# Optimization experiments

Hardware: AMD Instinct MI355X
Metric: run time of the kernel (lower is better)

Reference implementation:

```python
import jax, jax.numpy as jnp
import numpy as np

WL_W = 8   # wl_weight
WL_IN = 8  # wl_activate (input quantization)
EPS = 1e-5

def _wq(x, bits):
    # WAGE-style uniform quantize-dequantize to `bits` bits in [-1+step, 1-step], STE passthrough
    step = 2.0 ** (1 - bits)
    q = jnp.clip(jnp.round(x / step) * step, -1.0 + step, 1.0 - step)
    return x + jax.lax.stop_gradient(q - x)

def _qconv(x, w, b, pad):
    y = jax.lax.conv_general_dilated(
        _wq(x, WL_IN), _wq(w, WL_W), (1, 1), [(pad, pad), (pad, pad)],
        dimension_numbers=('NCHW', 'OIHW', 'NCHW'))
    return y + b[None, :, None, None]

def _bn_relu(x, g, be):
    # BatchNorm2d in training mode: batch statistics over (N, H, W)
    m = jnp.mean(x, axis=(0, 2, 3), keepdims=True)
    v = jnp.var(x, axis=(0, 2, 3), keepdims=True)
    return jax.nn.relu((x - m) * jax.lax.rsqrt(v + EPS) * g[None, :, None, None] + be[None, :, None, None])

def _maxpool3(x):
    # MaxPool2d(3, stride=1, padding=1)
    return jax.lax.reduce_window(x, -jnp.inf, jax.lax.max,
                                 (1, 1, 3, 3), (1, 1, 1, 1),
                                 [(0, 0), (0, 0), (1, 1), (1, 1)])

def setup_inputs() -> dict:
    key = jax.random.key(0)
    ks = jax.random.split(key, 8)
    d = {'x': jax.random.normal(ks[0], (128, 192, 32, 32), jnp.float32)}
    specs = [('b1', 1, 64, 192, 1), ('b2a', 2, 96, 192, 1), ('b2b', 3, 128, 96, 3),
             ('b3a', 4, 16, 192, 1), ('b3b', 5, 32, 16, 3), ('b3c', 6, 32, 32, 3),
             ('b4', 7, 32, 192, 1)]
    for name, i, co, ci, k in specs:
        d[name + '_w'] = jax.random.normal(ks[i], (co, ci, k, k), jnp.float32) * 0.05
        d[name + '_b'] = jnp.zeros((co,), jnp.float32)
        d[name + '_g'] = jnp.ones((co,), jnp.float32)
        d[name + '_be'] = jnp.zeros((co,), jnp.float32)
    return d

def reference(x,
              b1_w, b1_b, b1_g, b1_be,
              b2a_w, b2a_b, b2a_g, b2a_be,
              b2b_w, b2b_b, b2b_g, b2b_be,
              b3a_w, b3a_b, b3a_g, b3a_be,
              b3b_w, b3b_b, b3b_g, b3b_be,
              b3c_w, b3c_b, b3c_g, b3c_be,
              b4_w, b4_b, b4_g, b4_be):
    y1 = _bn_relu(_qconv(x, b1_w, b1_b, 0), b1_g, b1_be)
    y2 = _bn_relu(_qconv(x, b2a_w, b2a_b, 0), b2a_g, b2a_be)
    y2 = _bn_relu(_qconv(y2, b2b_w, b2b_b, 1), b2b_g, b2b_be)
    y3 = _bn_relu(_qconv(x, b3a_w, b3a_b, 0), b3a_g, b3a_be)
    y3 = _bn_relu(_qconv(y3, b3b_w, b3b_b, 1), b3b_g, b3b_be)
    y3 = _bn_relu(_qconv(y3, b3c_w, b3c_b, 1), b3c_g, b3c_be)
    y4 = _bn_relu(_qconv(_maxpool3(x), b4_w, b4_b, 0), b4_g, b4_be)
    return jnp.concatenate([y1, y2, y3, y4], axis=1)  # [N, 256, 32, 32]
```

## Files before the change

kernel.cpp:

```cpp
#include <hip/hip_runtime.h>

typedef unsigned short u16;
typedef unsigned int u32;
typedef __attribute__((ext_vector_type(4))) int i32x4;
typedef __attribute__((ext_vector_type(4))) float f32x4;
typedef __attribute__((ext_vector_type(4))) u16 u16x4;
typedef __attribute__((ext_vector_type(8))) u16 u16x8;

#define PTOT 131072
#define NREP 16

static __device__ __forceinline__ int qi8(float v) {
  int q = (int)rintf(v * 128.f);
  return max(-127, min(127, q));
}
static __device__ __forceinline__ u16 bf_rne(float v) {
  u32 u = __float_as_uint(v);
  u += 0x7fffu + ((u >> 16) & 1u);
  return (u16)(u >> 16);
}
static __device__ __forceinline__ float bf2f(u16 v) {
  return __uint_as_float((u32)v << 16);
}

struct WPtrs { const float* p[7]; };

__global__ void wpack_kernel(WPtrs wp, char* __restrict__ o) {
  static const int S[7][5] = {
      {0,      192, 192, 1, 64},
      {12288,  192, 192, 1, 96},
      {30720,  96,  320, 3, 128},
      {153600, 192, 192, 1, 16},
      {156672, 16,  64,  3, 32},
      {162816, 32,  128, 3, 32},
      {175104, 192, 192, 1, 32},
  };
  int idx = blockIdx.x * 256 + threadIdx.x;
  if (idx >= 181248) return;
  int s = 0;
#pragma unroll
  for (int i = 1; i < 7; ++i)
    if (idx >= S[i][0]) s = i;
  int local = idx - S[s][0];
  int CIr = S[s][1], KROWP = S[s][2], KH = S[s][3], Co = S[s][4];
  int j = local & 15, lane = (local >> 4) & 63, f = local >> 10;
  int NF = Co >> 4;
  int c = f / NF, nf = f - c * NF;
  int co = nf * 16 + (lane & 15);
  int k = c * 64 + ((lane >> 4) << 4) + j;
  int r = k / KROWP, kk = k - r * KROWP;
  char val = 0;
  if (kk < 3 * CIr || KH == 1) {
    int kw = (KH == 1) ? 0 : (kk / CIr);
    int ci = (KH == 1) ? kk : (kk - kw * CIr);
    val = (char)qi8(wp.p[s][(((size_t)co * CIr + ci) * KH + r) * KH + kw]);
  }
  o[idx] = val;
}

__global__ __launch_bounds__(256) void quantx_kernel(const float* __restrict__ x,
                                                     char* __restrict__ xq) {
  __shared__ __align__(16) char tile[64][80];
  int n = blockIdx.z, hwb = blockIdx.x * 64, cb = blockIdx.y * 64;
  int lane = threadIdx.x & 63, sub = threadIdx.x >> 6;
#pragma unroll
  for (int i = 0; i < 16; ++i) {
    int c = sub + i * 4;
    float v = x[(((size_t)n * 192 + cb + c) << 10) + hwb + lane];
    tile[lane][c] = (char)qi8(v);
  }
  __syncthreads();
  int t = threadIdx.x, px = t >> 2, c16 = t & 3;
  uint4 v = *(const uint4*)&tile[px][c16 * 16];
  *(uint4*)&xq[(((size_t)n << 10) + hwb + px) * 192 + cb + c16 * 16] = v;
}

__global__ __launch_bounds__(256) void pool_kernel(const char* __restrict__ xq,
                                                   char* __restrict__ xpq) {
  int idx = blockIdx.x * 256 + threadIdx.x;
  int c16 = idx % 12;
  int p = idx / 12;
  int n = p >> 10, hw = p & 1023, h = hw >> 5, w = hw & 31;
  int m[16];
#pragma unroll
  for (int j = 0; j < 16; ++j) m[j] = -127;
  for (int dh = -1; dh <= 1; ++dh) {
    int hh = h + dh; if (hh < 0 || hh > 31) continue;
    for (int dw = -1; dw <= 1; ++dw) {
      int ww = w + dw; if (ww < 0 || ww > 31) continue;
      uint4 v = *(const uint4*)&xq[((((size_t)n << 5) + hh) * 32 + ww) * 192 + c16 * 16];
      const char* bb = reinterpret_cast<const char*>(&v);
#pragma unroll
      for (int t = 0; t < 16; ++t) {
        int b = (int)bb[t];
        m[t] = b > m[t] ? b : m[t];
      }
    }
  }
  uint4 o;
  char* ob = reinterpret_cast<char*>(&o);
#pragma unroll
  for (int t = 0; t < 16; ++t) ob[t] = (char)m[t];
  *(uint4*)&xpq[(size_t)p * 192 + c16 * 16] = o;
}

template <int NFW, int MF>
static __device__ __forceinline__ void conv_epilogue(
    i32x4 (&acc)[MF][NFW], int nfw, int lane, int wave, int mbase,
    u16* __restrict__ yh, double* __restrict__ stb, int ststride) {
  float yv[MF][NFW][4];
#pragma unroll
  for (int mf = 0; mf < MF; ++mf)
#pragma unroll
    for (int nf = 0; nf < NFW; ++nf)
      if (nf < nfw) {
        int col = nf * 16 + (lane & 15);
        int pix = mbase + mf * 16 + ((lane >> 4) << 2);
        u16x4 o;
#pragma unroll
        for (int r = 0; r < 4; ++r) {
          float v = (float)acc[mf][nf][r] * 6.103515625e-05f;
          yv[mf][nf][r] = v;
          o[r] = bf_rne(v);
        }
        *(u16x4*)&yh[(size_t)col * PTOT + pix] = o;
      }

  float s1[NFW], s2[NFW];
#pragma unroll
  for (int nf = 0; nf < NFW; ++nf) { s1[nf] = 0.f; s2[nf] = 0.f; }
#pragma unroll
  for (int mf = 0; mf < MF; ++mf)
#pragma unroll
    for (int nf = 0; nf < NFW; ++nf)
      if (nf < nfw)
#pragma unroll
        for (int r = 0; r < 4; ++r) {
          float v = yv[mf][nf][r];
          s1[nf] += v;
          s2[nf] += v * v;
        }
#pragma unroll
  for (int m = 16; m <= 32; m <<= 1)
#pragma unroll
    for (int nf = 0; nf < NFW; ++nf) {
      s1[nf] += __shfl_xor(s1[nf], m);
      s2[nf] += __shfl_xor(s2[nf], m);
    }
  __shared__ float red[4][NFW][16][2];
  if (lane < 16)
#pragma unroll
    for (int nf = 0; nf < NFW; ++nf) {
      red[wave][nf][lane][0] = s1[nf];
      red[wave][nf][lane][1] = s2[nf];
    }
  __syncthreads();
  const int t = threadIdx.x;
  if (t < 16 * nfw) {
    int nf = t >> 4, l = t & 15;
    float a = red[0][nf][l][0] + red[1][nf][l][0] + red[2][nf][l][0] + red[3][nf][l][0];
    float b = red[0][nf][l][1] + red[1][nf][l][1] + red[2][nf][l][1] + red[3][nf][l][1];
    int rep = blockIdx.x & (NREP - 1);
    atomicAdd(&stb[rep * ststride + 2 * t], (double)a);
    atomicAdd(&stb[rep * ststride + 2 * t + 1], (double)b);
  }
}

__global__ __launch_bounds__(256, 4) void cstat1x1_kernel(
    const char* __restrict__ xq, const char* __restrict__ xpq,
    const char* __restrict__ bpk, double* __restrict__ st, u16* __restrict__ yh) {
  constexpr int NFW = 6;
  constexpr int MF = 2;
  const int b = blockIdx.y;
  const int nfw = (b == 0) ? 4 : (b == 1) ? 6 : (b == 2) ? 1 : 2;
  const int bpo = (b == 0) ? 0 : (b == 1) ? 12288 : (b == 2) ? 153600 : 175104;
  const int sto = (b == 0) ? 0 : (b == 1) ? 256 * NREP
                           : (b == 2) ? 3 * 256 * NREP : 6 * 256 * NREP;
  const int yho = (b == 0) ? 0 : (b == 1) ? 64 : (b == 2) ? 160 : 176;
  const char* xin = (b == 3) ? xpq : xq;
  const char* bp = bpk + bpo;
  double* stb = st + sto;
  u16* yhb = yh + (size_t)yho * PTOT;

  const int lane = threadIdx.x & 63;
  const int wave = threadIdx.x >> 6;
  const int mbase = blockIdx.x * 128 + wave * 32;

  uint abase[MF];
#pragma unroll
  for (int mf = 0; mf < MF; ++mf)
    abase[mf] = (uint)(mbase + mf * 16 + (lane & 15)) * 192u;
  const uint klane = (uint)(lane >> 4) * 16u;
  const uint blane = (uint)lane * 16u;

  i32x4 acc[MF][NFW];
#pragma unroll
  for (int i = 0; i < MF; ++i)
#pragma unroll
    for (int j = 0; j < NFW; ++j) acc[i][j] = {0, 0, 0, 0};

#pragma unroll
  for (int c = 0; c < 3; ++c) {
    i32x4 af[MF];
#pragma unroll
    for (int mf = 0; mf < MF; ++mf)
      af[mf] = *(const i32x4*)(xin + (abase[mf] + (uint)c * 64u + klane));
    i32x4 bfr[NFW];
#pragma unroll
    for (int nf = 0; nf < NFW; ++nf)
      if (nf < nfw)
        bfr[nf] = *(const i32x4*)(bp + ((uint)((c * nfw + nf) * 1024) + blane));
#pragma unroll
    for (int mf = 0; mf < MF; ++mf)
#pragma unroll
      for (int nf = 0; nf < NFW; ++nf)
        if (nf < nfw)
          acc[mf][nf] = __builtin_amdgcn_mfma_i32_16x16x64_i8(af[mf], bfr[nf],
                                                              acc[mf][nf], 0, 0, 0);
  }

  conv_epilogue<NFW, MF>(acc, nfw, lane, wave, mbase, yhb, stb, 256);
}

template <int CI, int KROWP, int COB, int WPEU>
__global__ __launch_bounds__(256, WPEU) void cstat9q_kernel(
    const u16* __restrict__ yhin, const double* __restrict__ stp,
    const float* __restrict__ gp, const float* __restrict__ bep,
    const char* __restrict__ bp, int nft,
    double* __restrict__ stb, u16* __restrict__ yh) {
  constexpr int CPR = KROWP / 64;
  constexpr int NCH = 3 * CPR;
  constexpr int NFW = COB / 16;
  constexpr int MF = 2;
  constexpr int TILE = 6 * 34 * CI;

  __shared__ __align__(16) char atile[TILE + 64];
  __shared__ float2 cfl[CI];

  const int tid = threadIdx.x;

  if (tid < CI) {
    double s1d = 0., s2d = 0.;
#pragma unroll
    for (int r = 0; r < NREP; ++r) {
      s1d += stp[r * 256 + 2 * tid];
      s2d += stp[r * 256 + 2 * tid + 1];
    }
    double m = s1d * (1.0 / PTOT);
    double v = s2d * (1.0 / PTOT) - m * m;
    double inv = 1.0 / sqrt(v + 1e-5);
    double c0 = (double)gp[tid] * inv;
    cfl[tid] = make_float2((float)c0, (float)((double)bep[tid] - m * c0));
  }
  {
    uint4 z = {0, 0, 0, 0};
    for (int s = tid * 16; s < TILE + 64; s += 4096) *(uint4*)&atile[s] = z;
  }
  __syncthreads();

  const int p0 = blockIdx.x * 128;
  const int n = p0 >> 10, h0 = (p0 & 1023) >> 5;
  for (int task = tid; task < CI * 6; task += 256) {
    int co = task / 6, rr = task - co * 6;
    int irow = h0 - 1 + rr;
    if (irow < 0 || irow > 31) continue;
    const u16* src = yhin + (size_t)co * PTOT + (n << 10) + (irow << 5);
    float2 cc = cfl[co];
    char* dst = &atile[(rr * 34 + 1) * CI + co];
#pragma unroll
    for (int w8 = 0; w8 < 4; ++w8) {
      u16x8 v = *(const u16x8*)(src + w8 * 8);
#pragma unroll
      for (int e = 0; e < 8; ++e) {
        float z = fmaxf(fmaf(bf2f(v[e]), cc.x, cc.y), 0.f);
        dst[(w8 * 8 + e) * CI] = (char)min((int)rintf(z * 128.f), 127);
      }
    }
  }
  __syncthreads();

  const int lane = tid & 63;
  const int wave = tid >> 6;
  const int mbase = blockIdx.x * 128 + wave * 32;

  uint albase[MF];
#pragma unroll
  for (int mf = 0; mf < MF; ++mf) {
    int lp = wave * 32 + mf * 16 + (lane & 15);
    albase[mf] = (uint)((((lp >> 5) + 1) * 34 + 1 + (lp & 31)) * CI);
  }
  const uint klane = (uint)(lane >> 4) * 16u;
  const uint blane = (uint)lane * 16u;

  i32x4 acc[MF][NFW];
#pragma unroll
  for (int i = 0; i < MF; ++i)
#pragma unroll
    for (int j = 0; j < NFW; ++j) acc[i][j] = {0, 0, 0, 0};

#pragma unroll 2
  for (int c = 0; c < NCH; ++c) {
    int rr = c / CPR, o = (c - rr * CPR) * 64;
    uint koff = (uint)((rr - 1) * 34 * CI + o - CI);
    i32x4 af[MF];
#pragma unroll
    for (int mf = 0; mf < MF; ++mf)
      af[mf] = *(const i32x4*)&atile[albase[mf] + koff + klane];
    i32x4 bfr[NFW];
#pragma unroll
    for (int nf = 0; nf < NFW; ++nf)
      bfr[nf] = *(const i32x4*)(bp + ((uint)((c * nft + nf) * 1024) + blane));
#pragma unroll
    for (int mf = 0; mf < MF; ++mf)
#pragma unroll
      for (int nf = 0; nf < NFW; ++nf)
        acc[mf][nf] = __builtin_amdgcn_mfma_i32_16x16x64_i8(af[mf], bfr[nf],
                                                            acc[mf][nf], 0, 0, 0);
  }

  conv_epilogue<NFW, MF>(acc, NFW, lane, wave, mbase, yh, stb, 256);
}

struct BnPtrs { const float* g[4]; const float* be[4]; };

__global__ __launch_bounds__(256) void bnout_all_kernel(
    const u16* __restrict__ yh, const double* __restrict__ st, BnPtrs bp,
    float* __restrict__ out) {
  int co = blockIdx.y, chunk = blockIdx.x, tid = threadIdx.x;
  int br = (co < 64) ? 0 : (co < 192) ? 1 : (co < 224) ? 2 : 3;
  int lco = co - ((br == 0) ? 0 : (br == 1) ? 64 : (br == 2) ? 192 : 224);
  int yhoff = (br == 0) ? 0 : (br == 1) ? 208 : (br == 2) ? 368 : 176;
  int stoff = (br == 0) ? 0 : (br == 1) ? 2 * 256 * NREP
                         : (br == 2) ? 5 * 256 * NREP : 6 * 256 * NREP;
  const double* stb = st + stoff;
  double s1d = 0., s2d = 0.;
#pragma unroll
  for (int r = 0; r < NREP; ++r) {
    s1d += stb[r * 256 + 2 * lco];
    s2d += stb[r * 256 + 2 * lco + 1];
  }
  double m = s1d * (1.0 / PTOT);
  double v = s2d * (1.0 / PTOT) - m * m;
  double inv = 1.0 / sqrt(v + 1e-5);
  double c0d = (double)bp.g[br][lco] * inv;
  float c0 = (float)c0d;
  float c1 = (float)((double)bp.be[br][lco] - m * c0d);

  int p0 = chunk * 4096 + tid * 16;
  int n = p0 >> 10, hw = p0 & 1023;
  const u16* yp = yh + (size_t)(yhoff + lco) * PTOT + p0;
  float* op = out + (((size_t)(n * 256 + co)) << 10) + hw;
#pragma unroll
  for (int half = 0; half < 2; ++half) {
    u16x8 r = *(const u16x8*)(yp + half * 8);
    f32x4 a, b;
#pragma unroll
    for (int e = 0; e < 4; ++e) {
      a[e] = fmaxf(fmaf(bf2f(r[e]), c0, c1), 0.f);
      b[e] = fmaxf(fmaf(bf2f(r[e + 4]), c0, c1), 0.f);
    }
    *(f32x4*)(op + half * 8) = a;
    *(f32x4*)(op + half * 8 + 4) = b;
  }
}

extern "C" void kernel_launch(void* const* d_in, const int* in_sizes, int n_in,
                              void* d_out, int out_size, void* d_ws, size_t ws_size,
                              hipStream_t stream) {
  const float* x = (const float*)d_in[0];
  float* out = (float*)d_out;
  char* ws = (char*)d_ws;

  if (ws_size < 155599872ull) return;
  char* xq  = ws;
  char* xpq = ws + 25165824ull;
  u16* yh   = (u16*)(ws + 50331648ull);
  char* bpk = ws + 155189248ull;
  double* st = (double*)(ws + 155370496ull);

  hipMemsetAsync(st, 0, 7 * NREP * 256 * 8, stream);

  WPtrs wp;
  const int widx[7] = {1, 5, 9, 13, 17, 21, 25};
  for (int i = 0; i < 7; ++i) wp.p[i] = (const float*)d_in[widx[i]];
  wpack_kernel<<<708, 256, 0, stream>>>(wp, bpk);

  quantx_kernel<<<dim3(16, 3, 128), 256, 0, stream>>>(x, xq);
  pool_kernel<<<6144, 256, 0, stream>>>(xq, xpq);

  double* stB[7];
  for (int b = 0; b < 7; ++b) stB[b] = st + (size_t)b * NREP * 256;

  cstat1x1_kernel<<<dim3(1024, 4), 256, 0, stream>>>(xq, xpq, bpk, st, yh);

  cstat9q_kernel<96, 320, 128, 3><<<1024, 256, 0, stream>>>(
      yh + (size_t)64 * PTOT, stB[1], (const float*)d_in[7], (const float*)d_in[8],
      bpk + 30720, 8, stB[2], yh + (size_t)208 * PTOT);

  cstat9q_kernel<16, 64, 32, 4><<<1024, 256, 0, stream>>>(
      yh + (size_t)160 * PTOT, stB[3], (const float*)d_in[15], (const float*)d_in[16],
      bpk + 156672, 2, stB[4], yh + (size_t)336 * PTOT);

  cstat9q_kernel<32, 128, 32, 4><<<1024, 256, 0, stream>>>(
      yh + (size_t)336 * PTOT, stB[4], (const float*)d_in[19], (const float*)d_in[20],
      bpk + 162816, 2, stB[5], yh + (size_t)368 * PTOT);

  BnPtrs bp;
  bp.g[0] = (const float*)d_in[3];  bp.be[0] = (const float*)d_in[4];
  bp.g[1] = (const float*)d_in[11]; bp.be[1] = (const float*)d_in[12];
  bp.g[2] = (const float*)d_in[23]; bp.be[2] = (const float*)d_in[24];
  bp.g[3] = (const float*)d_in[27]; bp.be[3] = (const float*)d_in[28];
  bnout_all_kernel<<<dim3(32, 256), 256, 0, stream>>>(yh, st, bp, out);
}
```

Baseline: 206.9 us.

## Stage weights in LDS and retile the 3x3 b2b conv across waves

The 1x1 conv kernel and the small 3x3 conv kernels now copy their packed int8 weight fragments into shared memory once per block, instead of every wave reading them from global memory in the inner loop. A new dedicated kernel for the 96->128 3x3 conv splits the four waves into 2 pixel groups by 2 channel groups, each wave doing 4x4 MFMA tiles. That kernel has its own epilogue that reduces statistics across the paired waves. The aim is less redundant global/L2 weight traffic and better A/B fragment reuse per wave, at the cost of more LDS per block and more accumulator registers, which may lower occupancy.

```diff
diff --git a/kernel.cpp b/kernel.cpp
--- a/kernel.cpp
+++ b/kernel.cpp
@@ -171,6 +171,8 @@
     const char* __restrict__ bpk, double* __restrict__ st, u16* __restrict__ yh) {
   constexpr int NFW = 6;
   constexpr int MF = 2;
+  __shared__ __align__(16) char btile[18432];
+
   const int b = blockIdx.y;
   const int nfw = (b == 0) ? 4 : (b == 1) ? 6 : (b == 2) ? 1 : 2;
   const int bpo = (b == 0) ? 0 : (b == 1) ? 12288 : (b == 2) ? 153600 : 175104;
@@ -182,8 +184,14 @@
   double* stb = st + sto;
   u16* yhb = yh + (size_t)yho * PTOT;
 
-  const int lane = threadIdx.x & 63;
-  const int wave = threadIdx.x >> 6;
+  const int tid = threadIdx.x;
+  const int bsz = nfw * 3 * 1024;
+  for (int s = tid * 16; s < bsz; s += 4096)
+    *(uint4*)&btile[s] = *(const uint4*)(bp + s);
+  __syncthreads();
+
+  const int lane = tid & 63;
+  const int wave = tid >> 6;
   const int mbase = blockIdx.x * 128 + wave * 32;
 
   uint abase[MF];
@@ -209,7 +217,7 @@
 #pragma unroll
     for (int nf = 0; nf < NFW; ++nf)
       if (nf < nfw)
-        bfr[nf] = *(const i32x4*)(bp + ((uint)((c * nfw + nf) * 1024) + blane));
+        bfr[nf] = *(const i32x4*)&btile[(uint)((c * nfw + nf) * 1024) + blane];
 #pragma unroll
     for (int mf = 0; mf < MF; ++mf)
 #pragma unroll
@@ -222,8 +230,8 @@
   conv_epilogue<NFW, MF>(acc, nfw, lane, wave, mbase, yhb, stb, 256);
 }
 
-template <int CI, int KROWP, int COB, int WPEU>
-__global__ __launch_bounds__(256, WPEU) void cstat9q_kernel(
+template <int CI, int KROWP, int COB>
+__global__ __launch_bounds__(256, 4) void cstat9q_kernel(
     const u16* __restrict__ yhin, const double* __restrict__ stp,
     const float* __restrict__ gp, const float* __restrict__ bep,
     const char* __restrict__ bp, int nft,
@@ -233,8 +241,10 @@
   constexpr int NFW = COB / 16;
   constexpr int MF = 2;
   constexpr int TILE = 6 * 34 * CI;
+  constexpr int BSZ = NCH * NFW * 1024;
 
   __shared__ __align__(16) char atile[TILE + 64];
+  __shared__ __align__(16) char btile[BSZ];
   __shared__ float2 cfl[CI];
 
   const int tid = threadIdx.x;
@@ -252,6 +262,8 @@
     double c0 = (double)gp[tid] * inv;
     cfl[tid] = make_float2((float)c0, (float)((double)bep[tid] - m * c0));
   }
+  for (int s = tid * 16; s < BSZ; s += 4096)
+    *(uint4*)&btile[s] = *(const uint4*)(bp + s);
   {
     uint4 z = {0, 0, 0, 0};
     for (int s = tid * 16; s < TILE + 64; s += 4096) *(uint4*)&atile[s] = z;
@@ -309,7 +321,7 @@
     i32x4 bfr[NFW];
 #pragma unroll
     for (int nf = 0; nf < NFW; ++nf)
-      bfr[nf] = *(const i32x4*)(bp + ((uint)((c * nft + nf) * 1024) + blane));
+      bfr[nf] = *(const i32x4*)&btile[(uint)((c * nft + nf) * 1024) + blane];
 #pragma unroll
     for (int mf = 0; mf < MF; ++mf)
 #pragma unroll
@@ -319,6 +331,157 @@
   }
 
   conv_epilogue<NFW, MF>(acc, NFW, lane, wave, mbase, yh, stb, 256);
+}
+
+__global__ __launch_bounds__(256, 3) void cstat9q2_kernel(
+    const u16* __restrict__ yhin, const double* __restrict__ stp,
+    const float* __restrict__ gp, const float* __restrict__ bep,
+    const char* __restrict__ bp, double* __restrict__ stb, u16* __restrict__ yh) {
+  constexpr int CI = 96;
+  constexpr int CPR = 5;
+  constexpr int NCH = 15;
+  constexpr int MF = 4;
+  constexpr int NFW = 4;
+  constexpr int TILE = 6 * 34 * CI;
+
+  __shared__ __align__(16) char atile[TILE + 64];
+  __shared__ float2 cfl[CI];
+  __shared__ float red[4][NFW][16][2];
+
+  const int tid = threadIdx.x;
+
+  if (tid < CI) {
+    double s1d = 0., s2d = 0.;
+#pragma unroll
+    for (int r = 0; r < NREP; ++r) {
+      s1d += stp[r * 256 + 2 * tid];
+      s2d += stp[r * 256 + 2 * tid + 1];
+    }
+    double m = s1d * (1.0 / PTOT);
+    double v = s2d * (1.0 / PTOT) - m * m;
+    double inv = 1.0 / sqrt(v + 1e-5);
+    double c0 = (double)gp[tid] * inv;
+    cfl[tid] = make_float2((float)c0, (float)((double)bep[tid] - m * c0));
+  }
+  {
+    uint4 z = {0, 0, 0, 0};
+    for (int s = tid * 16; s < TILE + 64; s += 4096) *(uint4*)&atile[s] = z;
+  }
+  __syncthreads();
+
+  const int p0 = blockIdx.x * 128;
+  const int n = p0 >> 10, h0 = (p0 & 1023) >> 5;
+  for (int task = tid; task < CI * 6; task += 256) {
+    int co = task / 6, rr = task - co * 6;
+    int irow = h0 - 1 + rr;
+    if (irow < 0 || irow > 31) continue;
+    const u16* src = yhin + (size_t)co * PTOT + (n << 10) + (irow << 5);
+    float2 cc = cfl[co];
+    char* dst = &atile[(rr * 34 + 1) * CI + co];
+#pragma unroll
+    for (int w8 = 0; w8 < 4; ++w8) {
+      u16x8 v = *(const u16x8*)(src + w8 * 8);
+#pragma unroll
+      for (int e = 0; e < 8; ++e) {
+        float z = fmaxf(fmaf(bf2f(v[e]), cc.x, cc.y), 0.f);
+        dst[(w8 * 8 + e) * CI] = (char)min((int)rintf(z * 128.f), 127);
+      }
+    }
+  }
+  __syncthreads();
+
+  const int lane = tid & 63;
+  const int wave = tid >> 6;
+  const int pg = wave >> 1, cg = wave & 1;
+
+  uint albase[MF];
+#pragma unroll
+  for (int mf = 0; mf < MF; ++mf) {
+    int lp = pg * 64 + mf * 16 + (lane & 15);
+    albase[mf] = (uint)((((lp >> 5) + 1) * 34 + 1 + (lp & 31)) * CI);
+  }
+  const uint klane = (uint)(lane >> 4) * 16u;
+  const uint blane = (uint)lane * 16u;
+
+  i32x4 acc[MF][NFW];
+#pragma unroll
+  for (int i = 0; i < MF; ++i)
+#pragma unroll
+    for (int j = 0; j < NFW; ++j) acc[i][j] = {0, 0, 0, 0};
+
+#pragma unroll 3
+  for (int c = 0; c < NCH; ++c) {
+    int rr = c / CPR, o = (c - rr * CPR) * 64;
+    uint koff = (uint)((rr - 1) * 34 * CI + o - CI);
+    i32x4 af[MF];
+#pragma unroll
+    for (int mf = 0; mf < MF; ++mf)
+      af[mf] = *(const i32x4*)&atile[albase[mf] + koff + klane];
+    i32x4 bfr[NFW];
+#pragma unroll
+    for (int nf = 0; nf < NFW; ++nf)
+      bfr[nf] = *(const i32x4*)(bp + ((uint)((c * 8 + cg * 4 + nf) * 1024) + blane));
+#pragma unroll
+    for (int mf = 0; mf < MF; ++mf)
+#pragma unroll
+      for (int nf = 0; nf < NFW; ++nf)
+        acc[mf][nf] = __builtin_amdgcn_mfma_i32_16x16x64_i8(af[mf], bfr[nf],
+                                                            acc[mf][nf], 0, 0, 0);
+  }
+
+  float yv[MF][NFW][4];
+#pragma unroll
+  for (int mf = 0; mf < MF; ++mf)
+#pragma unroll
+    for (int nf = 0; nf < NFW; ++nf) {
+      int col = cg * 64 + nf * 16 + (lane & 15);
+      int pix = p0 + pg * 64 + mf * 16 + ((lane >> 4) << 2);
+      u16x4 o;
+#pragma unroll
+      for (int r = 0; r < 4; ++r) {
+        float v = (float)acc[mf][nf][r] * 6.103515625e-05f;
+        yv[mf][nf][r] = v;
+        o[r] = bf_rne(v);
+      }
+      *(u16x4*)&yh[(size_t)col * PTOT + pix] = o;
+    }
+
+  float s1[NFW], s2[NFW];
+#pragma unroll
+  for (int nf = 0; nf < NFW; ++nf) { s1[nf] = 0.f; s2[nf] = 0.f; }
+#pragma unroll
+  for (int mf = 0; mf < MF; ++mf)
+#pragma unroll
+    for (int nf = 0; nf < NFW; ++nf)
+#pragma unroll
+      for (int r = 0; r < 4; ++r) {
+        float v = yv[mf][nf][r];
+        s1[nf] += v;
+        s2[nf] += v * v;
+      }
+#pragma unroll
+  for (int m = 16; m <= 32; m <<= 1)
+#pragma unroll
+    for (int nf = 0; nf < NFW; ++nf) {
+      s1[nf] += __shfl_xor(s1[nf], m);
+      s2[nf] += __shfl_xor(s2[nf], m);
+    }
+  if (lane < 16)
+#pragma unroll
+    for (int nf = 0; nf < NFW; ++nf) {
+      red[wave][nf][lane][0] = s1[nf];
+      red[wave][nf][lane][1] = s2[nf];
+    }
+  __syncthreads();
+  if (tid < 128) {
+    int gch = tid >> 4, l = tid & 15;
+    int cg2 = gch >> 2, nf = gch & 3;
+    float a = red[cg2][nf][l][0] + red[2 + cg2][nf][l][0];
+    float b = red[cg2][nf][l][1] + red[2 + cg2][nf][l][1];
+    int rep = blockIdx.x & (NREP - 1);
+    atomicAdd(&stb[rep * 256 + 2 * tid], (double)a);
+    atomicAdd(&stb[rep * 256 + 2 * tid + 1], (double)b);
+  }
 }
 
 struct BnPtrs { const float* g[4]; const float* be[4]; };
@@ -393,15 +556,15 @@
 
   cstat1x1_kernel<<<dim3(1024, 4), 256, 0, stream>>>(xq, xpq, bpk, st, yh);
 
-  cstat9q_kernel<96, 320, 128, 3><<<1024, 256, 0, stream>>>(
+  cstat9q2_kernel<<<1024, 256, 0, stream>>>(
       yh + (size_t)64 * PTOT, stB[1], (const float*)d_in[7], (const float*)d_in[8],
-      bpk + 30720, 8, stB[2], yh + (size_t)208 * PTOT);
-
-  cstat9q_kernel<16, 64, 32, 4><<<1024, 256, 0, stream>>>(
+      bpk + 30720, stB[2], yh + (size_t)208 * PTOT);
+
+  cstat9q_kernel<16, 64, 32><<<1024, 256, 0, stream>>>(
       yh + (size_t)160 * PTOT, stB[3], (const float*)d_in[15], (const float*)d_in[16],
       bpk + 156672, 2, stB[4], yh + (size_t)336 * PTOT);
 
-  cstat9q_kernel<32, 128, 32, 4><<<1024, 256, 0, stream>>>(
+  cstat9q_kernel<32, 128, 32><<<1024, 256, 0, stream>>>(
       yh + (size_t)336 * PTOT, stB[4], (const float*)d_in[19], (const float*)d_in[20],
       bpk + 162816, 2, stB[5], yh + (size_t)368 * PTOT);
 
```

Measured after the change: 193.6 us. 6.4% less time.
